# Performance work log

Measured on AMD Instinct MI355X. Metric: run time of the kernel, lower is better.

The kernel has to match this reference:

```python
import jax
jax.config.update("jax_enable_x64", True)
import jax.numpy as jnp
import numpy as np

N_VALUES = 33_554_432   # flattened JaggedTensor values (e.g. 16K batch x 2K multi-hot)
ZCH_SIZE = 4_194_304    # number of managed-collision slots
ID_MAX = 2_147_483_647  # input_hash_size - 1


def setup_inputs() -> dict:
    key = jax.random.key(0)
    k1, k2, k3 = jax.random.split(key, 3)
    values = jax.random.randint(k1, (N_VALUES,), 0, ID_MAX, dtype=jnp.int64)
    mch_sorted_raw_ids = jnp.sort(
        jax.random.randint(k2, (ZCH_SIZE,), 0, ID_MAX, dtype=jnp.int64)
    )
    # remapped ids are a permutation of [0, zch_size)
    mch_remapped_ids_mapping = jax.random.permutation(
        k3, jnp.arange(ZCH_SIZE, dtype=jnp.int64)
    )
    return {
        "values": values,
        "mch_sorted_raw_ids": mch_sorted_raw_ids,
        "mch_remapped_ids_mapping": mch_remapped_ids_mapping,
        "zch_index": ZCH_SIZE,
    }


def reference(values, mch_sorted_raw_ids, mch_remapped_ids_mapping, zch_index):
    # torch.searchsorted default (right=False) == jnp side='left'.
    # Search over table[:-1] so gathered index is always in-bounds (matches torch code).
    searched_indices = jnp.searchsorted(
        mch_sorted_raw_ids[:-1], values, side="left"
    )
    retrieved = mch_sorted_raw_ids[searched_indices]          # gather [N]
    remapped = mch_remapped_ids_mapping[searched_indices]     # gather [N]
    # fused masked-scatter equivalent: hit -> remapped id, miss -> zch sentinel
    return jnp.where(retrieved == values, remapped, jnp.int64(zch_index))
```

## Files before the change

### kernel.cpp

```cpp
#include <hip/hip_runtime.h>


#define AUX_BITS 19
#define AUX_SH   (31 - AUX_BITS)
#define NBUCKET  (1u << AUX_BITS)
#define AUX_N    (NBUCKET + 1u)

typedef int vint4 __attribute__((ext_vector_type(4)));
typedef unsigned long long u64;

#define HK 2654435761u

__device__ __forceinline__ u64 sig_mask(unsigned v) {
    unsigned h = v * HK;
    return (1ULL << (h >> 26)) | (1ULL << ((h >> 20) & 63)) |
           (1ULL << ((h >> 14) & 63)) | (1ULL << ((h >> 8) & 63));
}

__global__ __launch_bounds__(256) void build_aux_scatter(
    const int* __restrict__ table, int m, int* __restrict__ aux) {
    int j = blockIdx.x * blockDim.x + threadIdx.x;
    if (j >= m) return;
    unsigned lo_k = (j == 0) ? 0u : ((((unsigned)table[j - 1]) >> AUX_SH) + 1u);
    unsigned hi_k = ((unsigned)table[j]) >> AUX_SH;
    for (unsigned k = lo_k; k <= hi_k; ++k) aux[k] = j;
    if (j == m - 1) {
        for (unsigned k = hi_k + 1; k <= NBUCKET; ++k) aux[k] = m;
    }
}

__global__ __launch_bounds__(256) void build_sigs(
    const int* __restrict__ table, const int* __restrict__ aux, int z,
    u64* __restrict__ filter) {
    unsigned k = blockIdx.x * blockDim.x + threadIdx.x;
    if (k >= NBUCKET) return;
    int p = aux[k];
    u64 sig = 0;
    while (p < z && ((((unsigned)table[p]) >> AUX_SH) == k)) {
        sig |= sig_mask((unsigned)table[p]);
        ++p;
    }
    filter[k] = sig;
}

__device__ __forceinline__ int resolve_window(
    int v, const int* __restrict__ table, const int* __restrict__ mapping,
    const int* __restrict__ aux, int z, int zch) {
    unsigned k = ((unsigned)v) >> AUX_SH;
    int lo = aux[k];
    int hi = aux[k + 1];
    int s = lo & ~3;
    int e = (hi + 3) & ~3;
    if (e > z) e = z;
    int cnt = 0;
    bool eq = false;
    for (int p = s; p < e; p += 4) {
        int4 t = *(const int4*)(table + p);
        cnt += (t.x < v) + (t.y < v) + (t.z < v) + (t.w < v);
        eq = eq | (t.x == v) | (t.y == v) | (t.z == v) | (t.w == v);
    }
    return eq ? mapping[s + cnt] : zch;
}

__global__ __launch_bounds__(256) void mch_remap_bloom_kernel(
    const vint4* __restrict__ values4,
    const int* __restrict__ table,
    const int* __restrict__ mapping,
    const int* __restrict__ zch_p,
    const int* __restrict__ aux,
    const u64* __restrict__ filter,
    vint4* __restrict__ out4,
    int half4, int z) {

    int zch = *zch_p;
    int i = blockIdx.x * blockDim.x + threadIdx.x;
    if (i >= half4) return;

    vint4 va = __builtin_nontemporal_load(values4 + i);
    vint4 vb = __builtin_nontemporal_load(values4 + i + half4);
    int v[8] = {va.x, va.y, va.z, va.w, vb.x, vb.y, vb.z, vb.w};

    u64 w[8];
#pragma unroll
    for (int e = 0; e < 8; ++e) w[e] = filter[((unsigned)v[e]) >> AUX_SH];

    int res[8];
#pragma unroll
    for (int e = 0; e < 8; ++e) {
        u64 mask = sig_mask((unsigned)v[e]);
        bool maybe = (w[e] & mask) == mask;
        res[e] = maybe ? resolve_window(v[e], table, mapping, aux, z, zch)
                       : zch;
    }
    vint4 oa, ob;
    oa.x = res[0]; oa.y = res[1]; oa.z = res[2]; oa.w = res[3];
    ob.x = res[4]; ob.y = res[5]; ob.z = res[6]; ob.w = res[7];
    __builtin_nontemporal_store(oa, out4 + i);
    __builtin_nontemporal_store(ob, out4 + i + half4);
}

__global__ __launch_bounds__(64) void mch_remap_tail_kernel(
    const int* __restrict__ values, const int* __restrict__ table,
    const int* __restrict__ mapping, const int* __restrict__ zch_p,
    const int* __restrict__ aux, const u64* __restrict__ filter,
    int* __restrict__ out, int start, int n, int z) {
    int i = start + blockIdx.x * blockDim.x + threadIdx.x;
    if (i >= n) return;
    int v = values[i];
    u64 w = filter[((unsigned)v) >> AUX_SH];
    u64 mask = sig_mask((unsigned)v);
    int zch = *zch_p;
    out[i] = ((w & mask) == mask)
                 ? resolve_window(v, table, mapping, aux, z, zch) : zch;
}

__global__ __launch_bounds__(256) void mch_remap_aux_kernel(
    const int* __restrict__ values, const int* __restrict__ table,
    const int* __restrict__ mapping, const int* __restrict__ zch_p,
    const int* __restrict__ aux, int* __restrict__ out, int n, int z) {
    int zch = *zch_p;
    int i = blockIdx.x * blockDim.x + threadIdx.x;
    if (i >= n) return;
    int v = __builtin_nontemporal_load(values + i);
    out[i] = resolve_window(v, table, mapping, aux, z, zch);
}

extern "C" void kernel_launch(void* const* d_in, const int* in_sizes, int n_in,
                              void* d_out, int out_size, void* d_ws, size_t ws_size,
                              hipStream_t stream) {
    const int* values  = (const int*)d_in[0];
    const int* table   = (const int*)d_in[1];
    const int* mapping = (const int*)d_in[2];
    const int* zch_p   = (const int*)d_in[3];
    int* out = (int*)d_out;

    int n = in_sizes[0];
    int z = in_sizes[1];
    int m = z - 1;

    size_t filter_bytes = (size_t)NBUCKET * 8;
    size_t aux_bytes    = (size_t)AUX_N * sizeof(int);
    int block = 256;

    if (ws_size >= filter_bytes + aux_bytes) {
        u64* filter = (u64*)d_ws;
        int* aux    = (int*)((char*)d_ws + filter_bytes);

        build_aux_scatter<<<(m + block - 1) / block, block, 0, stream>>>(
            table, m, aux);
        build_sigs<<<(NBUCKET + block - 1) / block, block, 0, stream>>>(
            table, aux, z, filter);

        int half4 = n >> 3;
        if (half4 > 0) {
            mch_remap_bloom_kernel<<<(half4 + block - 1) / block, block, 0, stream>>>(
                (const vint4*)values, table, mapping, zch_p, aux, filter,
                (vint4*)out, half4, z);
        }
        int done = (half4 << 3);
        if (done < n) {
            mch_remap_tail_kernel<<<((n - done) + 63) / 64, 64, 0, stream>>>(
                values, table, mapping, zch_p, aux, filter, out, done, n, z);
        }
    } else if (ws_size >= aux_bytes) {
        int* aux = (int*)d_ws;
        build_aux_scatter<<<(m + block - 1) / block, block, 0, stream>>>(
            table, m, aux);
        mch_remap_aux_kernel<<<(n + block - 1) / block, block, 0, stream>>>(
            values, table, mapping, zch_p, aux, out, n, z);
    }
}
```

Before: 504.3 us.

## Pack bucket base and blocked Bloom filter into one 16-byte record per cell

Replaces the separate 64-bit per-bucket Bloom signature and aux index array with a combined 16-byte record per cell. Each record holds the bucket's table base offset plus three 32-bit filter words, and a hash picks which word to test. The bucket count halves. A filter hit now needs no second aux lookup, and the window scan stops early once a table entry reaches or passes the query. The cost is a larger record footprint with more keys per cell. That may raise the false-positive rate, and the hit path now uses non-temporal loads for table and mapping.

```diff
diff --git a/kernel.cpp b/kernel.cpp
--- a/kernel.cpp
+++ b/kernel.cpp
@@ -1,52 +1,153 @@
 #include <hip/hip_runtime.h>
 
 
-#define AUX_BITS 19
-#define AUX_SH   (31 - AUX_BITS)
-#define NBUCKET  (1u << AUX_BITS)
-#define AUX_N    (NBUCKET + 1u)
+#define CELL_BITS 18
+#define CELL_SH   (31 - CELL_BITS)
+#define NCELL     (1u << CELL_BITS)
+#define AUXN      (NCELL + 1u)
 
 typedef int vint4 __attribute__((ext_vector_type(4)));
-typedef unsigned long long u64;
-
-#define HK 2654435761u
-
-__device__ __forceinline__ u64 sig_mask(unsigned v) {
-    unsigned h = v * HK;
-    return (1ULL << (h >> 26)) | (1ULL << ((h >> 20) & 63)) |
-           (1ULL << ((h >> 14) & 63)) | (1ULL << ((h >> 8) & 63));
+
+__device__ __forceinline__ void hash4(unsigned v, int* sel, unsigned* mask) {
+    unsigned h1 = v * 2654435761u;
+    unsigned h2 = v * 0x85EBCA6Bu;
+    *mask = (1u << (h1 & 31)) | (1u << ((h1 >> 5) & 31)) |
+            (1u << ((h1 >> 10) & 31)) | (1u << ((h1 >> 15) & 31));
+    *sel = (int)(((h2 >> 16) * 3u) >> 16);
 }
 
 __global__ __launch_bounds__(256) void build_aux_scatter(
     const int* __restrict__ table, int m, int* __restrict__ aux) {
     int j = blockIdx.x * blockDim.x + threadIdx.x;
     if (j >= m) return;
-    unsigned lo_k = (j == 0) ? 0u : ((((unsigned)table[j - 1]) >> AUX_SH) + 1u);
-    unsigned hi_k = ((unsigned)table[j]) >> AUX_SH;
+    unsigned lo_k = (j == 0) ? 0u : ((((unsigned)table[j - 1]) >> CELL_SH) + 1u);
+    unsigned hi_k = ((unsigned)table[j]) >> CELL_SH;
     for (unsigned k = lo_k; k <= hi_k; ++k) aux[k] = j;
     if (j == m - 1) {
-        for (unsigned k = hi_k + 1; k <= NBUCKET; ++k) aux[k] = m;
-    }
-}
-
-__global__ __launch_bounds__(256) void build_sigs(
+        for (unsigned k = hi_k + 1; k <= NCELL; ++k) aux[k] = m;
+    }
+}
+
+__global__ __launch_bounds__(256) void build_records(
     const int* __restrict__ table, const int* __restrict__ aux, int z,
-    u64* __restrict__ filter) {
+    vint4* __restrict__ rec) {
     unsigned k = blockIdx.x * blockDim.x + threadIdx.x;
-    if (k >= NBUCKET) return;
-    int p = aux[k];
-    u64 sig = 0;
-    while (p < z && ((((unsigned)table[p]) >> AUX_SH) == k)) {
-        sig |= sig_mask((unsigned)table[p]);
+    if (k >= NCELL) return;
+    int base = aux[k];
+    unsigned s0 = 0, s1 = 0, s2 = 0;
+    int p = base;
+    while (p < z) {
+        unsigned tv = (unsigned)__builtin_nontemporal_load(table + p);
+        if ((tv >> CELL_SH) != k) break;
+        int sel; unsigned mk;
+        hash4(tv, &sel, &mk);
+        s0 |= (sel == 0) ? mk : 0u;
+        s1 |= (sel == 1) ? mk : 0u;
+        s2 |= (sel == 2) ? mk : 0u;
         ++p;
     }
-    filter[k] = sig;
-}
-
-__device__ __forceinline__ int resolve_window(
-    int v, const int* __restrict__ table, const int* __restrict__ mapping,
-    const int* __restrict__ aux, int z, int zch) {
-    unsigned k = ((unsigned)v) >> AUX_SH;
+    vint4 r;
+    r.x = base; r.y = (int)s0; r.z = (int)s1; r.w = (int)s2;
+    rec[k] = r;
+}
+
+__device__ __forceinline__ int resolve_from_base(
+    int v, int base, const int* __restrict__ table,
+    const int* __restrict__ mapping, int z, int zch) {
+    int s = base & ~3;
+    int cnt = 0;
+    bool eq = false;
+    int p = s;
+    for (;;) {
+        if (p + 4 <= z) {
+            int tx = __builtin_nontemporal_load(table + p);
+            int ty = __builtin_nontemporal_load(table + p + 1);
+            int tz = __builtin_nontemporal_load(table + p + 2);
+            int tw = __builtin_nontemporal_load(table + p + 3);
+            cnt += (tx < v) + (ty < v) + (tz < v) + (tw < v);
+            eq = eq | (tx == v) | (ty == v) | (tz == v) | (tw == v);
+            p += 4;
+            if (tw >= v) break;
+        } else {
+            for (; p < z; ++p) {
+                int t = __builtin_nontemporal_load(table + p);
+                cnt += (t < v);
+                eq = eq | (t == v);
+            }
+            break;
+        }
+    }
+    return eq ? __builtin_nontemporal_load(mapping + (s + cnt)) : zch;
+}
+
+__global__ __launch_bounds__(256) void mch_remap_rec_kernel(
+    const vint4* __restrict__ values4,
+    const int* __restrict__ table,
+    const int* __restrict__ mapping,
+    const int* __restrict__ zch_p,
+    const vint4* __restrict__ rec,
+    vint4* __restrict__ out4,
+    int half4, int z) {
+
+    int zch = *zch_p;
+    int i = blockIdx.x * blockDim.x + threadIdx.x;
+    if (i >= half4) return;
+
+    vint4 va = __builtin_nontemporal_load(values4 + i);
+    vint4 vb = __builtin_nontemporal_load(values4 + i + half4);
+    int v[8] = {va.x, va.y, va.z, va.w, vb.x, vb.y, vb.z, vb.w};
+
+    vint4 r[8];
+#pragma unroll
+    for (int e = 0; e < 8; ++e) r[e] = rec[((unsigned)v[e]) >> CELL_SH];
+
+    int res[8];
+#pragma unroll
+    for (int e = 0; e < 8; ++e) {
+        int sel; unsigned mk;
+        hash4((unsigned)v[e], &sel, &mk);
+        unsigned w = (sel == 0) ? (unsigned)r[e].y
+                   : (sel == 1) ? (unsigned)r[e].z
+                                : (unsigned)r[e].w;
+        bool maybe = (w & mk) == mk;
+        res[e] = maybe
+                     ? resolve_from_base(v[e], r[e].x, table, mapping, z, zch)
+                     : zch;
+    }
+    vint4 oa, ob;
+    oa.x = res[0]; oa.y = res[1]; oa.z = res[2]; oa.w = res[3];
+    ob.x = res[4]; ob.y = res[5]; ob.z = res[6]; ob.w = res[7];
+    __builtin_nontemporal_store(oa, out4 + i);
+    __builtin_nontemporal_store(ob, out4 + i + half4);
+}
+
+__global__ __launch_bounds__(64) void mch_remap_tail_kernel(
+    const int* __restrict__ values, const int* __restrict__ table,
+    const int* __restrict__ mapping, const int* __restrict__ zch_p,
+    const vint4* __restrict__ rec, int* __restrict__ out,
+    int start, int n, int z) {
+    int i = start + blockIdx.x * blockDim.x + threadIdx.x;
+    if (i >= n) return;
+    int v = values[i];
+    vint4 r = rec[((unsigned)v) >> CELL_SH];
+    int sel; unsigned mk;
+    hash4((unsigned)v, &sel, &mk);
+    unsigned w = (sel == 0) ? (unsigned)r.y
+               : (sel == 1) ? (unsigned)r.z : (unsigned)r.w;
+    int zch = *zch_p;
+    out[i] = ((w & mk) == mk)
+                 ? resolve_from_base(v, r.x, table, mapping, z, zch) : zch;
+}
+
+__global__ __launch_bounds__(256) void mch_remap_aux_kernel(
+    const int* __restrict__ values, const int* __restrict__ table,
+    const int* __restrict__ mapping, const int* __restrict__ zch_p,
+    const int* __restrict__ aux, int* __restrict__ out, int n, int z) {
+    int zch = *zch_p;
+    int i = blockIdx.x * blockDim.x + threadIdx.x;
+    if (i >= n) return;
+    int v = __builtin_nontemporal_load(values + i);
+    unsigned k = ((unsigned)v) >> CELL_SH;
     int lo = aux[k];
     int hi = aux[k + 1];
     int s = lo & ~3;
@@ -59,70 +160,7 @@
         cnt += (t.x < v) + (t.y < v) + (t.z < v) + (t.w < v);
         eq = eq | (t.x == v) | (t.y == v) | (t.z == v) | (t.w == v);
     }
-    return eq ? mapping[s + cnt] : zch;
-}
-
-__global__ __launch_bounds__(256) void mch_remap_bloom_kernel(
-    const vint4* __restrict__ values4,
-    const int* __restrict__ table,
-    const int* __restrict__ mapping,
-    const int* __restrict__ zch_p,
-    const int* __restrict__ aux,
-    const u64* __restrict__ filter,
-    vint4* __restrict__ out4,
-    int half4, int z) {
-
-    int zch = *zch_p;
-    int i = blockIdx.x * blockDim.x + threadIdx.x;
-    if (i >= half4) return;
-
-    vint4 va = __builtin_nontemporal_load(values4 + i);
-    vint4 vb = __builtin_nontemporal_load(values4 + i + half4);
-    int v[8] = {va.x, va.y, va.z, va.w, vb.x, vb.y, vb.z, vb.w};
-
-    u64 w[8];
-#pragma unroll
-    for (int e = 0; e < 8; ++e) w[e] = filter[((unsigned)v[e]) >> AUX_SH];
-
-    int res[8];
-#pragma unroll
-    for (int e = 0; e < 8; ++e) {
-        u64 mask = sig_mask((unsigned)v[e]);
-        bool maybe = (w[e] & mask) == mask;
-        res[e] = maybe ? resolve_window(v[e], table, mapping, aux, z, zch)
-                       : zch;
-    }
-    vint4 oa, ob;
-    oa.x = res[0]; oa.y = res[1]; oa.z = res[2]; oa.w = res[3];
-    ob.x = res[4]; ob.y = res[5]; ob.z = res[6]; ob.w = res[7];
-    __builtin_nontemporal_store(oa, out4 + i);
-    __builtin_nontemporal_store(ob, out4 + i + half4);
-}
-
-__global__ __launch_bounds__(64) void mch_remap_tail_kernel(
-    const int* __restrict__ values, const int* __restrict__ table,
-    const int* __restrict__ mapping, const int* __restrict__ zch_p,
-    const int* __restrict__ aux, const u64* __restrict__ filter,
-    int* __restrict__ out, int start, int n, int z) {
-    int i = start + blockIdx.x * blockDim.x + threadIdx.x;
-    if (i >= n) return;
-    int v = values[i];
-    u64 w = filter[((unsigned)v) >> AUX_SH];
-    u64 mask = sig_mask((unsigned)v);
-    int zch = *zch_p;
-    out[i] = ((w & mask) == mask)
-                 ? resolve_window(v, table, mapping, aux, z, zch) : zch;
-}
-
-__global__ __launch_bounds__(256) void mch_remap_aux_kernel(
-    const int* __restrict__ values, const int* __restrict__ table,
-    const int* __restrict__ mapping, const int* __restrict__ zch_p,
-    const int* __restrict__ aux, int* __restrict__ out, int n, int z) {
-    int zch = *zch_p;
-    int i = blockIdx.x * blockDim.x + threadIdx.x;
-    if (i >= n) return;
-    int v = __builtin_nontemporal_load(values + i);
-    out[i] = resolve_window(v, table, mapping, aux, z, zch);
+    out[i] = eq ? mapping[s + cnt] : zch;
 }
 
 extern "C" void kernel_launch(void* const* d_in, const int* in_sizes, int n_in,
@@ -138,29 +176,29 @@
     int z = in_sizes[1];
     int m = z - 1;
 
-    size_t filter_bytes = (size_t)NBUCKET * 8;
-    size_t aux_bytes    = (size_t)AUX_N * sizeof(int);
+    size_t rec_bytes = (size_t)NCELL * 16;
+    size_t aux_bytes = (size_t)AUXN * sizeof(int);
     int block = 256;
 
-    if (ws_size >= filter_bytes + aux_bytes) {
-        u64* filter = (u64*)d_ws;
-        int* aux    = (int*)((char*)d_ws + filter_bytes);
+    if (ws_size >= rec_bytes + aux_bytes) {
+        vint4* rec = (vint4*)d_ws;
+        int*   aux = (int*)((char*)d_ws + rec_bytes);
 
         build_aux_scatter<<<(m + block - 1) / block, block, 0, stream>>>(
             table, m, aux);
-        build_sigs<<<(NBUCKET + block - 1) / block, block, 0, stream>>>(
-            table, aux, z, filter);
+        build_records<<<(NCELL + block - 1) / block, block, 0, stream>>>(
+            table, aux, z, rec);
 
         int half4 = n >> 3;
         if (half4 > 0) {
-            mch_remap_bloom_kernel<<<(half4 + block - 1) / block, block, 0, stream>>>(
-                (const vint4*)values, table, mapping, zch_p, aux, filter,
+            mch_remap_rec_kernel<<<(half4 + block - 1) / block, block, 0, stream>>>(
+                (const vint4*)values, table, mapping, zch_p, rec,
                 (vint4*)out, half4, z);
         }
         int done = (half4 << 3);
         if (done < n) {
             mch_remap_tail_kernel<<<((n - done) + 63) / 64, 64, 0, stream>>>(
-                values, table, mapping, zch_p, aux, filter, out, done, n, z);
+                values, table, mapping, zch_p, rec, out, done, n, z);
         }
     } else if (ws_size >= aux_bytes) {
         int* aux = (int*)d_ws;
```

Result: slower. 673.2 us (+33.5%).
